# Optimization experiments

Hardware: AMD Instinct MI355X
Metric: run time of the kernel (lower is better)

## Reference

```python
import jax, jax.numpy as jnp
import numpy as np
import math

B, S, H, E, TOPK, NHEADS = 8, 512, 1024, 8, 2, 8
CAP = int(B * S * 1.5 * TOPK / E)  # 1536


def _linear(x, w, b):
    # torch nn.Linear convention: y = x @ w.T + b, w: [out, in]
    return x @ w.T + b


def _mha(x, in_w, in_b, out_w, out_b, n_heads):
    # torch nn.MultiheadAttention self-attention, eval mode (no dropout)
    Bx, Sx, D = x.shape
    dh = D // n_heads
    qkv = x @ in_w.T + in_b                      # [B,S,3D]
    q, k, v = jnp.split(qkv, 3, axis=-1)
    def heads(t):
        return t.reshape(Bx, Sx, n_heads, dh).transpose(0, 2, 1, 3)  # [B,h,S,dh]
    q, k, v = heads(q), heads(k), heads(v)
    scores = jnp.einsum('bhqd,bhkd->bhqk', q, k) / math.sqrt(dh)
    attn = jax.nn.softmax(scores, axis=-1)
    o = jnp.einsum('bhqk,bhkd->bhqd', attn, v)   # [B,h,S,dh]
    o = o.transpose(0, 2, 1, 3).reshape(Bx, Sx, D)
    return o @ out_w.T + out_b


def setup_inputs() -> dict:
    key = jax.random.key(0)
    ks = jax.random.split(key, 24)
    sc = 0.02
    d = {
        'hidden_states': jax.random.normal(ks[0], (B, S, H), jnp.float32),
        'pos_emb': jax.random.normal(ks[1], (S, H), jnp.float32) * sc,
        'se_w1': jax.random.normal(ks[2], (H // 4, 1), jnp.float32) * sc,
        'se_b1': jnp.zeros((H // 4,), jnp.float32),
        'se_w2': jax.random.normal(ks[3], (H // 4, H // 4), jnp.float32) * sc,
        'se_b2': jnp.zeros((H // 4,), jnp.float32),
        'sexp_w': jax.random.normal(ks[4], (H, H // 4), jnp.float32) * sc,
        'sexp_b': jnp.zeros((H,), jnp.float32),
        'te_w1': jax.random.normal(ks[5], (H, H + 2), jnp.float32) * sc,
        'te_b1': jnp.zeros((H,), jnp.float32),
        'te_w2': jax.random.normal(ks[6], (H, H), jnp.float32) * sc,
        'te_b2': jnp.zeros((H,), jnp.float32),
        'attn_in_w': jax.random.normal(ks[7], (3 * H, H), jnp.float32) * sc,
        'attn_in_b': jnp.zeros((3 * H,), jnp.float32),
        'attn_out_w': jax.random.normal(ks[8], (H, H), jnp.float32) * sc,
        'attn_out_b': jnp.zeros((H,), jnp.float32),
        'tr_w1': jax.random.normal(ks[9], (H, H), jnp.float32) * sc,
        'tr_b1': jnp.zeros((H,), jnp.float32),
        'tr_w2': jax.random.normal(ks[10], (E, H), jnp.float32) * sc,
        'tr_b2': jnp.zeros((E,), jnp.float32),
    }
    return d


def reference(hidden_states, pos_emb, se_w1, se_b1, se_w2, se_b2, sexp_w, sexp_b,
              te_w1, te_b1, te_w2, te_b2, attn_in_w, attn_in_b, attn_out_w, attn_out_b,
              tr_w1, tr_b1, tr_w2, tr_b2):
    b, s, h = hidden_states.shape
    timestamps = jnp.arange(s, dtype=hidden_states.dtype)           # [S]
    seasonality = jnp.sin(timestamps * 2 * jnp.pi / 24)             # [S]
    ts_b = jnp.broadcast_to(timestamps, (b, s))
    se_b = jnp.broadcast_to(seasonality, (b, s))

    position_embeddings = pos_emb[:s][None]                          # [1,S,H]
    seas = jax.nn.relu(_linear(se_b[..., None], se_w1, se_b1))       # [B,S,H/4]
    seas = _linear(seas, se_w2, se_b2)
    seasonal_embeddings = _linear(seas, sexp_w, sexp_b)              # [B,S,H]

    time_features = jnp.stack([ts_b, se_b], axis=-1)                 # [B,S,2]
    combined = jnp.concatenate([hidden_states, time_features], -1)   # [B,S,H+2]
    enc = jax.nn.relu(_linear(combined, te_w1, te_b1))
    enc = _linear(enc, te_w2, te_b2)
    enc = enc + position_embeddings + seasonal_embeddings
    enc = _mha(enc, attn_in_w, attn_in_b, attn_out_w, attn_out_b, NHEADS)

    logits = _linear(jax.nn.relu(_linear(enc, tr_w1, tr_b1)), tr_w2, tr_b2)  # [B,S,E]
    router_probs = jax.nn.softmax(logits, axis=-1)
    top_k_probs, top_k_idx = jax.lax.top_k(router_probs, TOPK)
    top_k_probs = top_k_probs / top_k_probs.sum(-1, keepdims=True)

    capacity = int(b * s * 1.5 * TOPK / E)
    # top-k indices are distinct per token, so summed one-hots replicate the
    # python loop's slot-0 writes exactly.
    onehot = jax.nn.one_hot(top_k_idx, E, dtype=router_probs.dtype)  # [B,S,K,E]
    disp0 = onehot.sum(axis=2)                                        # [B,S,E]
    comb0 = jnp.einsum('bske,bsk->bse', onehot, top_k_probs)          # [B,S,E]
    dispatch = jnp.zeros((b, s, E, capacity), router_probs.dtype).at[:, :, :, 0].set(disp0)
    combine = jnp.zeros((b, s, E, capacity), router_probs.dtype).at[:, :, :, 0].set(comb0)

    p_mean = router_probs.mean(axis=(0, 1))
    aux_loss = jnp.sum(p_mean * jnp.log(p_mean * E + 1e-9))
    return dispatch, combine, router_probs, aux_loss
```

## Files before the change

kernel.cpp:

```cpp
#include <hip/hip_runtime.h>
#include <hip/hip_bf16.h>


#define Hh 1024

typedef __attribute__((ext_vector_type(8))) short short8v;
typedef __attribute__((ext_vector_type(4))) float f32x4;

static __device__ __forceinline__ ushort f2bf(float x) {
  uint u = __float_as_uint(x);
  u += 0x7FFF + ((u >> 16) & 1);
  return (ushort)(u >> 16);
}
static __device__ __forceinline__ float bf2f(ushort h) {
  return __uint_as_float(((uint)h) << 16);
}

template<int EPI, bool RELU, bool HAS_BN, bool HAS_BSN>
__global__ __launch_bounds__(256, 2) void mgemm_k(
    const ushort* __restrict__ A, int lda, long long sAmaj, long long sAmin, int aHi, int aLo,
    const ushort* __restrict__ Bf, int BNT, int BKC, long long sBmaj, long long sBmin,
    float* __restrict__ Cf, ushort* __restrict__ Ch, int ldc, long long sCmaj, long long sCmin,
    int splitOff,
    ushort* __restrict__ pK, ushort* __restrict__ pV,
    int Kd, int zdiv,
    const float* __restrict__ bN, const float* __restrict__ bSN, int ldbs, int smod,
    float alpha)
{
  int gx = gridDim.x, gy = gridDim.y;
  int lin = (blockIdx.z * gy + blockIdx.y) * gx + blockIdx.x;
  int nwg = gx * gy * gridDim.z;
  int cpx = nwg >> 3;
  int swz = (lin & 7) * cpx + (lin >> 3);
  int bz = swz / (gx * gy);
  int rem = swz - bz * (gx * gy);
  int by = rem / gx, bx = rem - by * gx;

  int zj = bz / zdiv, zi = bz - zj * zdiv;
  A += (size_t)zj * sAmaj + (size_t)zi * sAmin;
  const ushort* bfb = Bf + (size_t)zj * sBmaj + (size_t)zi * sBmin;
  long long coff = (long long)zj * sCmaj + (long long)zi * sCmin;

  int m0 = by * 128, n0 = bx * 128;

  __shared__ __align__(16) ushort smem[16384];

  int t = threadIdx.x;
  int l = t & 63, w = t >> 6;
  int wm = w >> 1, wn = w & 1;

  f32x4 acc[4][4];
#pragma unroll
  for (int i = 0; i < 4; ++i)
#pragma unroll
    for (int j = 0; j < 4; ++j) acc[i][j] = (f32x4){0.f, 0.f, 0.f, 0.f};

  int srow = t >> 1;
  int sc = (t & 1) * 2;
  const ushort* gAh = A + (size_t)(m0 + srow) * lda + aHi + sc * 8;
  const ushort* gAl = A + (size_t)(m0 + srow) * lda + aLo + sc * 8;
  int wsw = ((srow >> 1) & 7) << 4;
  int wo0 = (srow * 64 + sc * 16) ^ wsw;
  int wo1 = wo0 ^ 16;

  int aoff[4];
#pragma unroll
  for (int mi = 0; mi < 4; ++mi) {
    int row = wm * 64 + mi * 16 + (l & 15);
    aoff[mi] = (row * 64 + (l >> 4) * 16) ^ (((row >> 1) & 7) << 4);
  }

  const ushort* bph[4];
  const ushort* bpl[4];
  int ntg0 = (n0 >> 4) + wn * 4;
#pragma unroll
  for (int ni = 0; ni < 4; ++ni) {
    bph[ni] = bfb + ((size_t)(ntg0 + ni) * BKC) * 512 + l * 8;
    bpl[ni] = bfb + ((size_t)(BNT + ntg0 + ni) * BKC) * 512 + l * 8;
  }

  int4 a0h0, a0h1, a0l0, a0l1, a1h0, a1h1, a1l0, a1l1;
  short8v B0h[4], B0l[4], B1h[4], B1l[4];

#define LOADA0(s) { a0h0 = *(const int4*)(gAh + (s)*32); a0h1 = *(const int4*)(gAh + (s)*32 + 8); \
                    a0l0 = *(const int4*)(gAl + (s)*32); a0l1 = *(const int4*)(gAl + (s)*32 + 8); }
#define LOADA1(s) { a1h0 = *(const int4*)(gAh + (s)*32); a1h1 = *(const int4*)(gAh + (s)*32 + 8); \
                    a1l0 = *(const int4*)(gAl + (s)*32); a1l1 = *(const int4*)(gAl + (s)*32 + 8); }
#define STOREA(h0, h1, l0, l1, base) { char* nb = (char*)smem + (base); \
    *(int4*)(nb + wo0) = h0; *(int4*)(nb + wo1) = h1; \
    *(int4*)(nb + 8192 + wo0) = l0; *(int4*)(nb + 8192 + wo1) = l1; }
#define LOADB(BH, BL, s) { _Pragma("unroll") \
    for (int ni = 0; ni < 4; ++ni) { \
      BH[ni] = *(const short8v*)(bph[ni] + (size_t)(s) * 512); \
      BL[ni] = *(const short8v*)(bpl[ni] + (size_t)(s) * 512); } }
#define MFMA_STEP(ahb, alb, BH, BL) { \
    short8v ah[4], al[4]; \
    _Pragma("unroll") for (int mi = 0; mi < 4; ++mi) \
      ah[mi] = *(const short8v*)((char*)smem + (ahb) + aoff[mi]); \
    _Pragma("unroll") for (int mi = 0; mi < 4; ++mi) \
      al[mi] = *(const short8v*)((char*)smem + (alb) + aoff[mi]); \
    _Pragma("unroll") for (int ni = 0; ni < 4; ++ni) \
      _Pragma("unroll") for (int mi = 0; mi < 4; ++mi) \
        acc[mi][ni] = __builtin_amdgcn_mfma_f32_16x16x32_bf16(ah[mi], BH[ni], acc[mi][ni], 0, 0, 0); \
    _Pragma("unroll") for (int ni = 0; ni < 4; ++ni) \
      _Pragma("unroll") for (int mi = 0; mi < 4; ++mi) \
        acc[mi][ni] = __builtin_amdgcn_mfma_f32_16x16x32_bf16(al[mi], BH[ni], acc[mi][ni], 0, 0, 0); \
    _Pragma("unroll") for (int ni = 0; ni < 4; ++ni) \
      _Pragma("unroll") for (int mi = 0; mi < 4; ++mi) \
        acc[mi][ni] = __builtin_amdgcn_mfma_f32_16x16x32_bf16(ah[mi], BL[ni], acc[mi][ni], 0, 0, 0); }

  int nt = Kd >> 5;
  LOADA0(0); LOADB(B0h, B0l, 0);
  LOADA1(1); LOADB(B1h, B1l, 1);
  STOREA(a0h0, a0h1, a0l0, a0l1, 0);
  __syncthreads();
  for (int s2 = 0; s2 < nt; s2 += 2) {
    if (s2 + 2 < nt) LOADA0(s2 + 2);
    MFMA_STEP(0, 8192, B0h, B0l);
    if (s2 + 2 < nt) LOADB(B0h, B0l, s2 + 2);
    STOREA(a1h0, a1h1, a1l0, a1l1, 16384);
    __syncthreads();
    if (s2 + 3 < nt) LOADA1(s2 + 3);
    MFMA_STEP(16384, 24576, B1h, B1l);
    if (s2 + 3 < nt) LOADB(B1h, B1l, s2 + 3);
    if (s2 + 2 < nt) STOREA(a0h0, a0h1, a0l0, a0l1, 0);
    __syncthreads();
  }
#undef LOADA0
#undef LOADA1
#undef STOREA
#undef LOADB
#undef MFMA_STEP

#pragma unroll
  for (int mi = 0; mi < 4; ++mi)
#pragma unroll
    for (int j = 0; j < 4; ++j) {
      int m = m0 + wm * 64 + mi * 16 + (l >> 4) * 4 + j;
#pragma unroll
      for (int ni = 0; ni < 4; ++ni) {
        int n = n0 + wn * 64 + ni * 16 + (l & 15);
        float x = acc[mi][ni][j] * alpha;
        if (HAS_BN) x += bN[n];
        if (HAS_BSN) x += bSN[(size_t)(m % smod) * ldbs + n];
        if (RELU) x = fmaxf(x, 0.f);
        acc[mi][ni][j] = x;
      }
    }

  if (EPI == 0) {
    float* Fs = (float*)smem;
#pragma unroll
    for (int p = 0; p < 2; ++p) {
      __syncthreads();
      if (wm == p) {
#pragma unroll
        for (int mi = 0; mi < 4; ++mi)
#pragma unroll
          for (int j = 0; j < 4; ++j) {
            int r = mi * 16 + (l >> 4) * 4 + j;
#pragma unroll
            for (int ni = 0; ni < 4; ++ni) {
              int c = wn * 64 + ni * 16 + (l & 15);
              *(float*)((char*)Fs + ((r * 512 + c * 4) ^ ((r & 7) << 4))) = acc[mi][ni][j];
            }
          }
      }
      __syncthreads();
#pragma unroll
      for (int r8 = 0; r8 < 8; ++r8) {
        int idx = r8 * 256 + t;
        int row = idx >> 5, slot = idx & 31;
        int4 v = *(const int4*)((char*)Fs + ((row * 512 + slot * 16) ^ ((row & 7) << 4)));
        *(int4*)(Cf + coff + (size_t)(m0 + p * 64 + row) * ldc + n0 + slot * 4) = v;
      }
    }
  } else {
    __syncthreads();
    ushort* Es = smem;
    bool isQ = (EPI == 1) || (n0 < 1024);
    bool isK = (EPI == 2) && !isQ && (n0 < 2048);
    int bb = m0 >> 9, s0 = m0 & 511;
    int hh2 = isK ? ((n0 - 1024) >> 7) : ((n0 - 2048) >> 7);
    size_t kvb = (size_t)(bb * 8 + hh2) * 131072;
#pragma unroll
    for (int pass = 0; pass < 2; ++pass) {
      if (!(EPI == 2 && !isQ && !isK)) {
#pragma unroll
        for (int mi = 0; mi < 4; ++mi)
#pragma unroll
          for (int j = 0; j < 4; ++j) {
            int lr = wm * 64 + mi * 16 + (l >> 4) * 4 + j;
#pragma unroll
            for (int ni = 0; ni < 4; ++ni) {
              int lcb = (wn * 64 + ni * 16 + (l & 15)) * 2;
              float x = acc[mi][ni][j];
              ushort h = f2bf(x);
              ushort vv = (pass == 0) ? h : f2bf(x - bf2f(h));
              *(ushort*)((char*)Es + ((lr * 256 + lcb) ^ ((lr & 7) << 4))) = vv;
            }
          }
      } else {
#pragma unroll
        for (int mi = 0; mi < 4; ++mi)
#pragma unroll
          for (int j = 0; j < 4; ++j) {
            int cc = (wm * 64 + mi * 16 + (l >> 4) * 4 + j) * 2;
#pragma unroll
            for (int ni = 0; ni < 4; ++ni) {
              int rr = wn * 64 + ni * 16 + (l & 15);
              float x = acc[mi][ni][j];
              ushort h = f2bf(x);
              ushort vv = (pass == 0) ? h : f2bf(x - bf2f(h));
              *(ushort*)((char*)Es + ((rr * 256 + cc) ^ ((rr & 7) << 4))) = vv;
            }
          }
      }
      __syncthreads();
      if (isQ) {
        int off = (pass == 0) ? 0 : splitOff;
#pragma unroll
        for (int r = 0; r < 8; ++r) {
          int idx = r * 256 + t;
          int row = idx >> 4, cb = (idx & 15) * 16;
          int4 v = *(const int4*)((char*)Es + ((row * 256 + cb) ^ ((row & 7) << 4)));
          *(int4*)((char*)(Ch + coff + (size_t)(m0 + row) * ldc + off + n0) + cb) = v;
        }
      } else if (isK) {
#pragma unroll
        for (int sw = 0; sw < 8; ++sw) {
          int idx = sw * 256 + t;
          int f = idx >> 6, l2 = idx & 63;
          int st = f >> 2, dc = f & 3;
          int row = st * 16 + (l2 & 15);
          int colB = (dc * 32 + ((l2 >> 4) << 3)) * 2;
          short8v v = *(const short8v*)((char*)Es + ((row * 256 + colB) ^ ((row & 7) << 4)));
          *(short8v*)(pK + kvb + (size_t)((pass * 32 + (s0 >> 4) + st) * 4 + dc) * 512 + l2 * 8) = v;
        }
      } else {
#pragma unroll
        for (int sw = 0; sw < 8; ++sw) {
          int idx = sw * 256 + t;
          int f = idx >> 6, l2 = idx & 63;
          int dt = f >> 2, sch = f & 3;
          int row = dt * 16 + (l2 & 15);
          int colB = (sch * 32 + ((l2 >> 4) << 3)) * 2;
          short8v v = *(const short8v*)((char*)Es + ((row * 256 + colB) ^ ((row & 7) << 4)));
          *(short8v*)(pV + kvb + (size_t)((pass * 8 + dt) * 16 + (s0 >> 5) + sch) * 512 + l2 * 8) = v;
        }
      }
      if (pass == 0) __syncthreads();
    }
  }
}

__global__ __launch_bounds__(512, 2) void attn_k(
    const ushort* __restrict__ qbuf, const ushort* __restrict__ Kf,
    const ushort* __restrict__ Vf, ushort* __restrict__ attno)
{
  int qt = blockIdx.x;
  int bh = blockIdx.y;
  int b = bh >> 3, h = bh & 7;

  __shared__ __align__(16) ushort smem[32768];
  __shared__ float rowred[1024];

  int t = threadIdx.x;
  int l = t & 63, w = t >> 6;
  int wm = w >> 2, wn = w & 3;

  {
    int srow = t >> 2, sc = t & 3;
    const ushort* gQ = qbuf + (size_t)(b * 512 + qt * 128 + srow) * 2048 + h * 128 + sc * 8;
    int wo = (srow * 64 + sc * 16) ^ (((srow >> 1) & 7) << 4);
#pragma unroll
    for (int ks = 0; ks < 4; ++ks) {
      int4 vh = *(const int4*)(gQ + ks * 32);
      int4 vl = *(const int4*)(gQ + 1024 + ks * 32);
      *(int4*)((char*)smem + ks * 8192 + wo) = vh;
      *(int4*)((char*)smem + 32768 + ks * 8192 + wo) = vl;
    }
  }

  int aoff[4];
#pragma unroll
  for (int mi = 0; mi < 4; ++mi) {
    int row = wm * 64 + mi * 16 + (l & 15);
    aoff[mi] = (row * 64 + (l >> 4) * 16) ^ (((row >> 1) & 7) << 4);
  }

  __syncthreads();

  f32x4 S[4][4][2];
#pragma unroll
  for (int c = 0; c < 4; ++c)
#pragma unroll
    for (int mi = 0; mi < 4; ++mi)
#pragma unroll
      for (int ni = 0; ni < 2; ++ni) S[c][mi][ni] = (f32x4){0.f, 0.f, 0.f, 0.f};

  const ushort* Kb = Kf + (size_t)bh * 131072 + l * 8;
#pragma unroll
  for (int c = 0; c < 4; ++c) {
#pragma unroll
    for (int ks = 0; ks < 4; ++ks) {
      short8v bhf[2], blf[2], ahf[4], alf[4];
#pragma unroll
      for (int ni = 0; ni < 2; ++ni) {
        int ntk = c * 8 + wn * 2 + ni;
        bhf[ni] = *(const short8v*)(Kb + (size_t)(ntk * 4 + ks) * 512);
        blf[ni] = *(const short8v*)(Kb + (size_t)((32 + ntk) * 4 + ks) * 512);
      }
#pragma unroll
      for (int mi = 0; mi < 4; ++mi) {
        ahf[mi] = *(const short8v*)((char*)smem + ks * 8192 + aoff[mi]);
        alf[mi] = *(const short8v*)((char*)smem + 32768 + ks * 8192 + aoff[mi]);
      }
#pragma unroll
      for (int ni = 0; ni < 2; ++ni)
#pragma unroll
        for (int mi = 0; mi < 4; ++mi)
          S[c][mi][ni] = __builtin_amdgcn_mfma_f32_16x16x32_bf16(ahf[mi], bhf[ni], S[c][mi][ni], 0, 0, 0);
#pragma unroll
      for (int ni = 0; ni < 2; ++ni)
#pragma unroll
        for (int mi = 0; mi < 4; ++mi)
          S[c][mi][ni] = __builtin_amdgcn_mfma_f32_16x16x32_bf16(alf[mi], bhf[ni], S[c][mi][ni], 0, 0, 0);
#pragma unroll
      for (int ni = 0; ni < 2; ++ni)
#pragma unroll
        for (int mi = 0; mi < 4; ++mi)
          S[c][mi][ni] = __builtin_amdgcn_mfma_f32_16x16x32_bf16(ahf[mi], blf[ni], S[c][mi][ni], 0, 0, 0);
    }
  }

  const float scale = 0.08838834764831845f;
  float inv16[4][4];
  {
    float mx[4][4];
#pragma unroll
    for (int mi = 0; mi < 4; ++mi)
#pragma unroll
      for (int j = 0; j < 4; ++j) {
        float m2 = -3.0e38f;
#pragma unroll
        for (int c = 0; c < 4; ++c)
#pragma unroll
          for (int ni = 0; ni < 2; ++ni) m2 = fmaxf(m2, S[c][mi][ni][j]);
#pragma unroll
        for (int off = 8; off; off >>= 1) m2 = fmaxf(m2, __shfl_xor(m2, off));
        mx[mi][j] = m2;
      }
    if ((l & 15) == 0) {
#pragma unroll
      for (int mi = 0; mi < 4; ++mi)
#pragma unroll
        for (int j = 0; j < 4; ++j) {
          int row = wm * 64 + mi * 16 + (l >> 4) * 4 + j;
          rowred[wn * 128 + row] = mx[mi][j];
        }
    }
    __syncthreads();
#pragma unroll
    for (int mi = 0; mi < 4; ++mi)
#pragma unroll
      for (int j = 0; j < 4; ++j) {
        int row = wm * 64 + mi * 16 + (l >> 4) * 4 + j;
        float m2 = fmaxf(fmaxf(rowred[row], rowred[128 + row]),
                         fmaxf(rowred[256 + row], rowred[384 + row]));
        mx[mi][j] = m2 * scale;
      }
    float sm[4][4];
#pragma unroll
    for (int mi = 0; mi < 4; ++mi)
#pragma unroll
      for (int j = 0; j < 4; ++j) {
        float s2 = 0.f;
#pragma unroll
        for (int c = 0; c < 4; ++c)
#pragma unroll
          for (int ni = 0; ni < 2; ++ni) {
            float p = __expf(fmaf(S[c][mi][ni][j], scale, -mx[mi][j]));
            S[c][mi][ni][j] = p;
            s2 += p;
          }
#pragma unroll
        for (int off = 8; off; off >>= 1) s2 += __shfl_xor(s2, off);
        sm[mi][j] = s2;
      }
    if ((l & 15) == 0) {
#pragma unroll
      for (int mi = 0; mi < 4; ++mi)
#pragma unroll
        for (int j = 0; j < 4; ++j) {
          int row = wm * 64 + mi * 16 + (l >> 4) * 4 + j;
          rowred[512 + wn * 128 + row] = sm[mi][j];
        }
    }
    __syncthreads();
#pragma unroll
    for (int mi = 0; mi < 4; ++mi)
#pragma unroll
      for (int j = 0; j < 4; ++j) {
        int row = wm * 64 + mi * 16 + (l >> 4) * 4 + j;
        float s2 = rowred[512 + row] + rowred[640 + row]
                 + rowred[768 + row] + rowred[896 + row];
        inv16[mi][j] = 1.f / s2;
      }
  }

  f32x4 O[4][2];
#pragma unroll
  for (int mi = 0; mi < 4; ++mi)
#pragma unroll
    for (int ni = 0; ni < 2; ++ni) O[mi][ni] = (f32x4){0.f, 0.f, 0.f, 0.f};

  const ushort* Vb = Vf + (size_t)bh * 131072 + l * 8;
#pragma unroll
  for (int c = 0; c < 4; ++c) {
    __syncthreads();
#pragma unroll
    for (int mi = 0; mi < 4; ++mi)
#pragma unroll
      for (int j = 0; j < 4; ++j) {
        int row = wm * 64 + mi * 16 + (l >> 4) * 4 + j;
        int sw2 = ((row >> 1) & 7) << 4;
#pragma unroll
        for (int ni = 0; ni < 2; ++ni) {
          float p = S[c][mi][ni][j] * inv16[mi][j];
          ushort hh = f2bf(p);
          ushort ll2 = f2bf(p - bf2f(hh));
          int off = (row * 64 + (ni * 16 + (l & 15)) * 2) ^ sw2;
          *(ushort*)((char*)smem + wn * 8192 + off) = hh;
          *(ushort*)((char*)smem + 32768 + wn * 8192 + off) = ll2;
        }
      }
    __syncthreads();
#pragma unroll
    for (int ks = 0; ks < 4; ++ks) {
      short8v pah[4], pal[4], vbh[2], vbl[2];
#pragma unroll
      for (int ni = 0; ni < 2; ++ni) {
        int ntd = wn * 2 + ni;
        vbh[ni] = *(const short8v*)(Vb + (size_t)(ntd * 16 + c * 4 + ks) * 512);
        vbl[ni] = *(const short8v*)(Vb + (size_t)((8 + ntd) * 16 + c * 4 + ks) * 512);
      }
#pragma unroll
      for (int mi = 0; mi < 4; ++mi) {
        pah[mi] = *(const short8v*)((char*)smem + ks * 8192 + aoff[mi]);
        pal[mi] = *(const short8v*)((char*)smem + 32768 + ks * 8192 + aoff[mi]);
      }
#pragma unroll
      for (int ni = 0; ni < 2; ++ni)
#pragma unroll
        for (int mi = 0; mi < 4; ++mi)
          O[mi][ni] = __builtin_amdgcn_mfma_f32_16x16x32_bf16(pah[mi], vbh[ni], O[mi][ni], 0, 0, 0);
#pragma unroll
      for (int ni = 0; ni < 2; ++ni)
#pragma unroll
        for (int mi = 0; mi < 4; ++mi)
          O[mi][ni] = __builtin_amdgcn_mfma_f32_16x16x32_bf16(pal[mi], vbh[ni], O[mi][ni], 0, 0, 0);
#pragma unroll
      for (int ni = 0; ni < 2; ++ni)
#pragma unroll
        for (int mi = 0; mi < 4; ++mi)
          O[mi][ni] = __builtin_amdgcn_mfma_f32_16x16x32_bf16(pah[mi], vbl[ni], O[mi][ni], 0, 0, 0);
    }
  }

  __syncthreads();
  ushort* Es = smem;
  size_t coff = (size_t)b * 1048576 + (size_t)h * 128;
  int m0 = qt * 128;
#pragma unroll
  for (int pass = 0; pass < 2; ++pass) {
#pragma unroll
    for (int mi = 0; mi < 4; ++mi)
#pragma unroll
      for (int j = 0; j < 4; ++j) {
        int lr = wm * 64 + mi * 16 + (l >> 4) * 4 + j;
#pragma unroll
        for (int ni = 0; ni < 2; ++ni) {
          int lcb = (wn * 32 + ni * 16 + (l & 15)) * 2;
          float x = O[mi][ni][j];
          ushort hh = f2bf(x);
          ushort vv = (pass == 0) ? hh : f2bf(x - bf2f(hh));
          *(ushort*)((char*)Es + ((lr * 256 + lcb) ^ ((lr & 7) << 4))) = vv;
        }
      }
    __syncthreads();
    int off = (pass == 0) ? 0 : 1024;
#pragma unroll
    for (int r = 0; r < 4; ++r) {
      int idx = r * 512 + t;
      int row = idx >> 4, cb = (idx & 15) * 16;
      int4 v = *(const int4*)((char*)Es + ((row * 256 + cb) ^ ((row & 7) << 4)));
      *(int4*)((char*)(attno + coff + (size_t)(m0 + row) * 2048 + off) + cb) = v;
    }
    if (pass == 0) __syncthreads();
  }
}

__global__ __launch_bounds__(64) void convall_k(
    const float* __restrict__ te_w1, const float* __restrict__ te_w2,
    const float* __restrict__ ain_w, const float* __restrict__ aout_w,
    const float* __restrict__ tr_w1, ushort* __restrict__ base)
{
  int kc = blockIdx.x, y = blockIdx.y, l = threadIdx.x;
  const float* W; int ldw, NT, nt2; ushort* dst;
  if (y < 64)       { W = te_w1;  ldw = 1026; NT = 64;  nt2 = y;       dst = base; }
  else if (y < 128) { W = te_w2;  ldw = 1024; NT = 64;  nt2 = y - 64;  dst = base + 2097152; }
  else if (y < 320) { W = ain_w;  ldw = 1024; NT = 192; nt2 = y - 128; dst = base + 4194304; }
  else if (y < 384) { W = aout_w; ldw = 1024; NT = 64;  nt2 = y - 320; dst = base + 10485760; }
  else              { W = tr_w1;  ldw = 1024; NT = 64;  nt2 = y - 384; dst = base + 12582912; }
  const float* src = W + (size_t)(nt2 * 16 + (l & 15)) * ldw + kc * 32 + ((l >> 4) << 3);
  ushort h8[8], l8[8];
#pragma unroll
  for (int j = 0; j < 8; ++j) {
    float x = src[j];
    h8[j] = f2bf(x);
    l8[j] = f2bf(x - bf2f(h8[j]));
  }
  *(int4*)(dst + ((size_t)nt2 * 32 + kc) * 512 + l * 8) = *(int4*)h8;
  *(int4*)(dst + ((size_t)(NT + nt2) * 32 + kc) * 512 + l * 8) = *(int4*)l8;
}

__global__ __launch_bounds__(256) void convert_k(
    const float* __restrict__ W, int lda, ushort* __restrict__ Whl, int K)
{
  int r = blockIdx.x;
  int c = threadIdx.x * 4;
  const float* src = W + (size_t)r * lda + c;
  float x0 = src[0], x1 = src[1], x2 = src[2], x3 = src[3];
  ushort4 h, lo;
  h.x = f2bf(x0); lo.x = f2bf(x0 - bf2f(h.x));
  h.y = f2bf(x1); lo.y = f2bf(x1 - bf2f(h.y));
  h.z = f2bf(x2); lo.z = f2bf(x2 - bf2f(h.z));
  h.w = f2bf(x3); lo.w = f2bf(x3 - bf2f(h.w));
  ushort* dst = Whl + (size_t)r * 2 * K;
  *(ushort4*)&dst[c] = h;
  *(ushort4*)&dst[K + c] = lo;
}

__global__ __launch_bounds__(256) void precompute_k(
    const float* __restrict__ pos_emb,
    const float* __restrict__ se_w1, const float* __restrict__ se_b1,
    const float* __restrict__ se_w2, const float* __restrict__ se_b2,
    const float* __restrict__ sexp_w, const float* __restrict__ sexp_b,
    const float* __restrict__ te_w1, const float* __restrict__ te_b1,
    float* __restrict__ psea, float* __restrict__ bias1)
{
  int s = blockIdx.x, t = threadIdx.x;
  float ts = (float)s;
  float se = sinf(((ts * 2.0f) * 3.14159274101257324f) / 24.0f);
  __shared__ float l1[256], l2[256];
  l1[t] = fmaxf(se * se_w1[t] + se_b1[t], 0.f);
  __syncthreads();
  {
    float a = se_b2[t];
    const float* wr = se_w2 + (size_t)t * 256;
    for (int i = 0; i < 256; ++i) a += l1[i] * wr[i];
    l2[t] = a;
  }
  __syncthreads();
#pragma unroll
  for (int r = 0; r < 4; ++r) {
    int h = r * 256 + t;
    float v = sexp_b[h];
    const float* wr = sexp_w + (size_t)h * 256;
    for (int j = 0; j < 256; ++j) v += l2[j] * wr[j];
    psea[s * Hh + h] = pos_emb[s * Hh + h] + v;
    bias1[s * Hh + h] = te_b1[h] + ts * te_w1[(size_t)h * 1026 + 1024]
                                 + se * te_w1[(size_t)h * 1026 + 1025];
  }
}

__global__ __launch_bounds__(256) void tr2_k(
    const float* __restrict__ h1, const float* __restrict__ w,
    const float* __restrict__ bias, float* __restrict__ logits)
{
  int wid = threadIdx.x >> 6, lane = threadIdx.x & 63;
  int t = blockIdx.x * 4 + wid;
  const float* x = h1 + (size_t)t * Hh;
  float acc[8];
#pragma unroll
  for (int e = 0; e < 8; ++e) acc[e] = 0.f;
  for (int k = lane; k < Hh; k += 64) {
    float xv = x[k];
#pragma unroll
    for (int e = 0; e < 8; ++e) acc[e] += xv * w[e * Hh + k];
  }
#pragma unroll
  for (int e = 0; e < 8; ++e) {
#pragma unroll
    for (int off = 32; off; off >>= 1) acc[e] += __shfl_xor(acc[e], off);
  }
  if (lane == 0) {
#pragma unroll
    for (int e = 0; e < 8; ++e) logits[(size_t)t * 8 + e] = acc[e] + bias[e];
  }
}

__global__ __launch_bounds__(256) void fill0_k(float4* __restrict__ p, long long n4)
{
  long long i = (long long)blockIdx.x * 256 + threadIdx.x;
  long long stride = (long long)gridDim.x * 256;
  float4 z = make_float4(0.f, 0.f, 0.f, 0.f);
  for (; i < n4; i += stride) p[i] = z;
}

__global__ __launch_bounds__(256) void router_k(
    float* __restrict__ out, float* __restrict__ partials)
{
  int t = blockIdx.x * 256 + threadIdx.x;
  float* lg = out + 100663296 + (size_t)t * 8;
  float p[8];
#pragma unroll
  for (int e = 0; e < 8; ++e) p[e] = lg[e];
  float m = p[0];
#pragma unroll
  for (int e = 1; e < 8; ++e) m = fmaxf(m, p[e]);
  float s = 0.f;
#pragma unroll
  for (int e = 0; e < 8; ++e) { p[e] = expf(p[e] - m); s += p[e]; }
  float inv = 1.f / s;
#pragma unroll
  for (int e = 0; e < 8; ++e) p[e] *= inv;
#pragma unroll
  for (int e = 0; e < 8; ++e) lg[e] = p[e];

  int i0 = 0; float v0 = p[0];
#pragma unroll
  for (int e = 1; e < 8; ++e) if (p[e] > v0) { v0 = p[e]; i0 = e; }
  int i1 = -1; float v1 = -1.f;
#pragma unroll
  for (int e = 0; e < 8; ++e) if (e != i0 && p[e] > v1) { v1 = p[e]; i1 = e; }
  float wn = 1.f / (v0 + v1);
  size_t db = (size_t)t * (8 * 1536);
  out[db + (size_t)i0 * 1536] = 1.f;
  out[db + (size_t)i1 * 1536] = 1.f;
  out[50331648 + db + (size_t)i0 * 1536] = v0 * wn;
  out[50331648 + db + (size_t)i1 * 1536] = v1 * wn;

  __shared__ float red[256];
#pragma unroll
  for (int e = 0; e < 8; ++e) {
    red[threadIdx.x] = p[e];
    __syncthreads();
    for (int st = 128; st; st >>= 1) {
      if (threadIdx.x < st) red[threadIdx.x] += red[threadIdx.x + st];
      __syncthreads();
    }
    if (threadIdx.x == 0) partials[blockIdx.x * 8 + e] = red[0];
    __syncthreads();
  }
}

__global__ __launch_bounds__(64) void aux_k(float* __restrict__ partials,
                                            float* __restrict__ out)
{
  int lane = threadIdx.x;
  float v = 0.f;
  if (lane < 8) {
    float s = 0.f;
    for (int b = 0; b < 16; ++b) s += partials[b * 8 + lane];
    float pm = s / 4096.f;
    v = pm * logf(pm * 8.f + 1e-9f);
  }
#pragma unroll
  for (int off = 4; off; off >>= 1) v += __shfl_xor(v, off);
  if (lane == 0) out[100696064] = v;
  partials[lane] = 0.f;
  partials[64 + lane] = 0.f;
}

extern "C" void kernel_launch(void* const* d_in, const int* in_sizes, int n_in,
                              void* d_out, int out_size, void* d_ws, size_t ws_size,
                              hipStream_t stream)
{
  const float* hidden = (const float*)d_in[0];
  const float* pos_emb = (const float*)d_in[1];
  const float* se_w1 = (const float*)d_in[2];
  const float* se_b1 = (const float*)d_in[3];
  const float* se_w2 = (const float*)d_in[4];
  const float* se_b2 = (const float*)d_in[5];
  const float* sexp_w = (const float*)d_in[6];
  const float* sexp_b = (const float*)d_in[7];
  const float* te_w1 = (const float*)d_in[8];
  const float* te_b1 = (const float*)d_in[9];
  const float* te_w2 = (const float*)d_in[10];
  const float* te_b2 = (const float*)d_in[11];
  const float* ain_w = (const float*)d_in[12];
  const float* ain_b = (const float*)d_in[13];
  const float* aout_w = (const float*)d_in[14];
  const float* aout_b = (const float*)d_in[15];
  const float* tr_w1 = (const float*)d_in[16];
  const float* tr_b1 = (const float*)d_in[17];
  const float* tr_w2 = (const float*)d_in[18];
  const float* tr_b2 = (const float*)d_in[19];
  float* out = (float*)d_out;

  char* arena = (char*)d_out;
  ushort* Wbase= (ushort*)(arena + 0);
  ushort* hid2 = (ushort*)(arena + 29360128);
  ushort* enc1 = (ushort*)(arena + 46137344);
  ushort* enc2 = (ushort*)(arena + 62914560);
  ushort* qbuf = (ushort*)(arena + 79691776);
  ushort* Kf   = (ushort*)(arena + 96468992);
  ushort* Vf   = (ushort*)(arena + 113246208);
  ushort* attno= (ushort*)(arena + 197132288);
  ushort* encf = (ushort*)(arena + 213909504);
  float*  h1   = (float*)(arena + 230686720);
  float*  psea = (float*)(arena + 247463936);
  float*  bias1= (float*)(arena + 249561088);
  float*  parts= out + 51380224;
  float*  lgts = out + 100663296;

  convall_k<<<dim3(32, 448), 64, 0, stream>>>(te_w1, te_w2, ain_w, aout_w, tr_w1, Wbase);
  convert_k<<<4096, 256, 0, stream>>>(hidden, 1024, hid2, 1024);
  precompute_k<<<512, 256, 0, stream>>>(pos_emb, se_w1, se_b1, se_w2, se_b2,
                                        sexp_w, sexp_b, te_w1, te_b1, psea, bias1);

  mgemm_k<1, true, false, true><<<dim3(8, 32, 1), 256, 0, stream>>>(
      hid2, 2048, 0, 0, 0, 1024,
      Wbase, 64, 32, 0, 0,
      nullptr, enc1, 2048, 0, 0, 1024, nullptr, nullptr,
      1024, 1, nullptr, bias1, 1024, 512, 1.f);

  mgemm_k<1, false, true, true><<<dim3(8, 32, 1), 256, 0, stream>>>(
      enc1, 2048, 0, 0, 0, 1024,
      Wbase + 2097152, 64, 32, 0, 0,
      nullptr, enc2, 2048, 0, 0, 1024, nullptr, nullptr,
      1024, 1, te_b2, psea, 1024, 512, 1.f);

  mgemm_k<2, false, true, false><<<dim3(24, 32, 1), 256, 0, stream>>>(
      enc2, 2048, 0, 0, 0, 1024,
      Wbase + 4194304, 192, 32, 0, 0,
      nullptr, qbuf, 2048, 0, 0, 1024, Kf, Vf,
      1024, 1, ain_b, nullptr, 1, 1, 1.f);

  attn_k<<<dim3(4, 64), 512, 0, stream>>>(qbuf, Kf, Vf, attno);

  mgemm_k<1, false, true, false><<<dim3(8, 32, 1), 256, 0, stream>>>(
      attno, 2048, 0, 0, 0, 1024,
      Wbase + 10485760, 64, 32, 0, 0,
      nullptr, encf, 2048, 0, 0, 1024, nullptr, nullptr,
      1024, 1, aout_b, nullptr, 1, 1, 1.f);

  mgemm_k<0, true, true, false><<<dim3(8, 32, 1), 256, 0, stream>>>(
      encf, 2048, 0, 0, 0, 1024,
      Wbase + 12582912, 64, 32, 0, 0,
      h1, nullptr, 1024, 0, 0, 0, nullptr, nullptr,
      1024, 1, tr_b1, nullptr, 1, 1, 1.f);

  tr2_k<<<1024, 256, 0, stream>>>(h1, tr_w2, tr_b2, lgts);

  fill0_k<<<4096, 256, 0, stream>>>((float4*)out, 25165824LL);

  router_k<<<16, 256, 0, stream>>>(out, parts);
  aux_k<<<1, 64, 0, stream>>>(parts, out);
}
```

Measured before the change: 460.4 us.

## Spread output zero-fill across GEMM, attention and router kernels as extra blocks

The separate zero-fill kernel for the large dispatch/combine output is split into 256KB chunks. Each chunk is written by extra workgroups appended to the grids of the GEMM, attention and tr2 kernels, using arena regions that are free at that point in the schedule. The intent is to overlap the memory-bound fill with compute-bound kernels instead of running it serially. The cost is extra grid blocks that compete for CUs, and a dependency on careful arena aliasing so no buffer that is still live gets zeroed.

```diff
diff --git a/kernel.cpp b/kernel.cpp
--- a/kernel.cpp
+++ b/kernel.cpp
@@ -14,6 +14,18 @@
 }
 static __device__ __forceinline__ float bf2f(ushort h) {
   return __uint_as_float(((uint)h) << 16);
+}
+
+static __device__ __forceinline__ void fill_chunk(char* fz, long long base,
+                                                  long long limit, long long id) {
+  long long zo = base + id * 262144LL;
+  if (zo < limit) {
+    long long n16 = (limit - zo) >> 4;
+    if (n16 > 16384) n16 = 16384;
+    float4* zp = (float4*)(fz + zo);
+    float4 zz = make_float4(0.f, 0.f, 0.f, 0.f);
+    for (long long i = threadIdx.x; i < n16; i += blockDim.x) zp[i] = zz;
+  }
 }
 
 template<int EPI, bool RELU, bool HAS_BN, bool HAS_BSN>
@@ -25,9 +37,17 @@
     ushort* __restrict__ pK, ushort* __restrict__ pV,
     int Kd, int zdiv,
     const float* __restrict__ bN, const float* __restrict__ bSN, int ldbs, int smod,
-    float alpha)
-{
-  int gx = gridDim.x, gy = gridDim.y;
+    float alpha,
+    char* __restrict__ fz, long long fzBase, long long fzLimit, int gemmGX)
+{
+  int gy = gridDim.y;
+  if ((int)blockIdx.x >= gemmGX) {
+    int fx = gridDim.x - gemmGX;
+    long long id = ((long long)blockIdx.z * gy + blockIdx.y) * fx + (blockIdx.x - gemmGX);
+    fill_chunk(fz, fzBase, fzLimit, id);
+    return;
+  }
+  int gx = gemmGX;
   int lin = (blockIdx.z * gy + blockIdx.y) * gx + blockIdx.x;
   int nwg = gx * gy * gridDim.z;
   int cpx = nwg >> 3;
@@ -256,8 +276,13 @@
 
 __global__ __launch_bounds__(512, 2) void attn_k(
     const ushort* __restrict__ qbuf, const ushort* __restrict__ Kf,
-    const ushort* __restrict__ Vf, ushort* __restrict__ attno)
-{
+    const ushort* __restrict__ Vf, ushort* __restrict__ attno,
+    char* __restrict__ fz, long long fzBase, long long fzLimit)
+{
+  if (blockIdx.x >= 4) {
+    fill_chunk(fz, fzBase, fzLimit, (long long)blockIdx.y);
+    return;
+  }
   int qt = blockIdx.x;
   int bh = blockIdx.y;
   int b = bh >> 3, h = bh & 7;
@@ -577,8 +602,16 @@
 
 __global__ __launch_bounds__(256) void tr2_k(
     const float* __restrict__ h1, const float* __restrict__ w,
-    const float* __restrict__ bias, float* __restrict__ logits)
-{
+    const float* __restrict__ bias, float* __restrict__ logits,
+    char* __restrict__ fz, long long baseA, long long limitA,
+    long long baseB, long long limitB, int nA)
+{
+  if ((int)blockIdx.x >= 1024) {
+    int id = blockIdx.x - 1024;
+    if (id < nA) fill_chunk(fz, baseA, limitA, id);
+    else fill_chunk(fz, baseB, limitB, id - nA);
+    return;
+  }
   int wid = threadIdx.x >> 6, lane = threadIdx.x & 63;
   int t = blockIdx.x * 4 + wid;
   const float* x = h1 + (size_t)t * Hh;
@@ -721,41 +754,49 @@
   precompute_k<<<512, 256, 0, stream>>>(pos_emb, se_w1, se_b1, se_w2, se_b2,
                                         sexp_w, sexp_b, te_w1, te_b1, psea, bias1);
 
-  mgemm_k<1, true, false, true><<<dim3(8, 32, 1), 256, 0, stream>>>(
+  mgemm_k<1, true, false, true><<<dim3(16, 32, 1), 256, 0, stream>>>(
       hid2, 2048, 0, 0, 0, 1024,
       Wbase, 64, 32, 0, 0,
       nullptr, enc1, 2048, 0, 0, 1024, nullptr, nullptr,
-      1024, 1, nullptr, bias1, 1024, 512, 1.f);
-
-  mgemm_k<1, false, true, true><<<dim3(8, 32, 1), 256, 0, stream>>>(
+      1024, 1, nullptr, bias1, 1024, 512, 1.f,
+      arena, 130023424LL, 197132288LL, 8);
+
+  mgemm_k<1, false, true, true><<<dim3(16, 32, 1), 256, 0, stream>>>(
       enc1, 2048, 0, 0, 0, 1024,
       Wbase + 2097152, 64, 32, 0, 0,
       nullptr, enc2, 2048, 0, 0, 1024, nullptr, nullptr,
-      1024, 1, te_b2, psea, 1024, 512, 1.f);
-
-  mgemm_k<2, false, true, false><<<dim3(24, 32, 1), 256, 0, stream>>>(
+      1024, 1, te_b2, psea, 1024, 512, 1.f,
+      arena, 251658240LL, 318767104LL, 8);
+
+  mgemm_k<2, false, true, false><<<dim3(32, 32, 1), 256, 0, stream>>>(
       enc2, 2048, 0, 0, 0, 1024,
       Wbase + 4194304, 192, 32, 0, 0,
       nullptr, qbuf, 2048, 0, 0, 1024, Kf, Vf,
-      1024, 1, ain_b, nullptr, 1, 1, 1.f);
-
-  attn_k<<<dim3(4, 64), 512, 0, stream>>>(qbuf, Kf, Vf, attno);
-
-  mgemm_k<1, false, true, false><<<dim3(8, 32, 1), 256, 0, stream>>>(
+      1024, 1, ain_b, nullptr, 1, 1, 1.f,
+      arena, 318767104LL, 385875968LL, 24);
+
+  attn_k<<<dim3(5, 64), 512, 0, stream>>>(qbuf, Kf, Vf, attno,
+                                          arena, 385875968LL, 402653184LL);
+
+  mgemm_k<1, false, true, false><<<dim3(14, 32, 1), 256, 0, stream>>>(
       attno, 2048, 0, 0, 0, 1024,
       Wbase + 10485760, 64, 32, 0, 0,
       nullptr, encf, 2048, 0, 0, 1024, nullptr, nullptr,
-      1024, 1, aout_b, nullptr, 1, 1, 1.f);
-
-  mgemm_k<0, true, true, false><<<dim3(8, 32, 1), 256, 0, stream>>>(
+      1024, 1, aout_b, nullptr, 1, 1, 1.f,
+      arena, 79691776LL, 130023424LL, 8);
+
+  mgemm_k<0, true, true, false><<<dim3(14, 32, 1), 256, 0, stream>>>(
       encf, 2048, 0, 0, 0, 1024,
       Wbase + 12582912, 64, 32, 0, 0,
       h1, nullptr, 1024, 0, 0, 0, nullptr, nullptr,
-      1024, 1, tr_b1, nullptr, 1, 1, 1.f);
-
-  tr2_k<<<1024, 256, 0, stream>>>(h1, tr_w2, tr_b2, lgts);
-
-  fill0_k<<<4096, 256, 0, stream>>>((float4*)out, 25165824LL);
+      1024, 1, tr_b1, nullptr, 1, 1, 1.f,
+      arena, 29360128LL, 79691776LL, 8);
+
+  tr2_k<<<1264, 256, 0, stream>>>(h1, tr_w2, tr_b2, lgts,
+                                  arena, 0LL, 29360128LL,
+                                  197132288LL, 230686720LL, 112);
+
+  fill0_k<<<80, 256, 0, stream>>>((float4*)(arena + 230686720), 1310720LL);
 
   router_k<<<16, 256, 0, stream>>>(out, parts);
   aux_k<<<1, 64, 0, stream>>>(parts, out);
```

Result: slower. 552.6 us (+20.0%).

## Double the GEMM K-tile to 64 to halve barriers per K step

Applied to the files above, without the earlier changes.

The split-bf16 GEMM mainloop now stages 64-wide K tiles of A (hi and lo) in LDS instead of 32-wide. It uses a new XOR swizzle and issues two MFMA sub-steps per barrier, so there is one __syncthreads per 64 K. This cuts synchronization and LDS store overhead per MFMA. In exchange it doubles LDS to 64KB per block and adds more A staging registers, which may reduce occupancy below the two-blocks-per-CU launch bound. It also assumes K is a multiple of 128.

```diff
diff --git a/kernel.cpp b/kernel.cpp
--- a/kernel.cpp
+++ b/kernel.cpp
@@ -43,7 +43,7 @@
 
   int m0 = by * 128, n0 = bx * 128;
 
-  __shared__ __align__(16) ushort smem[16384];
+  __shared__ __align__(16) ushort smem[32768];
 
   int t = threadIdx.x;
   int l = t & 63, w = t >> 6;
@@ -56,18 +56,21 @@
     for (int j = 0; j < 4; ++j) acc[i][j] = (f32x4){0.f, 0.f, 0.f, 0.f};
 
   int srow = t >> 1;
-  int sc = (t & 1) * 2;
-  const ushort* gAh = A + (size_t)(m0 + srow) * lda + aHi + sc * 8;
-  const ushort* gAl = A + (size_t)(m0 + srow) * lda + aLo + sc * 8;
-  int wsw = ((srow >> 1) & 7) << 4;
-  int wo0 = (srow * 64 + sc * 16) ^ wsw;
-  int wo1 = wo0 ^ 16;
-
-  int aoff[4];
+  int sc4 = (t & 1) * 4;
+  const ushort* gAh = A + (size_t)(m0 + srow) * lda + aHi + sc4 * 8;
+  const ushort* gAl = A + (size_t)(m0 + srow) * lda + aLo + sc4 * 8;
+  int woA[4];
+#pragma unroll
+  for (int i = 0; i < 4; ++i)
+    woA[i] = srow * 128 + (((sc4 + i) ^ (srow & 7)) << 4);
+
+  int aoff[4][2];
 #pragma unroll
   for (int mi = 0; mi < 4; ++mi) {
     int row = wm * 64 + mi * 16 + (l & 15);
-    aoff[mi] = (row * 64 + (l >> 4) * 16) ^ (((row >> 1) & 7) << 4);
+#pragma unroll
+    for (int kk = 0; kk < 2; ++kk)
+      aoff[mi][kk] = row * 128 + ((((kk << 2) + (l >> 4)) ^ (row & 7)) << 4);
   }
 
   const ushort* bph[4];
@@ -79,26 +82,29 @@
     bpl[ni] = bfb + ((size_t)(BNT + ntg0 + ni) * BKC) * 512 + l * 8;
   }
 
-  int4 a0h0, a0h1, a0l0, a0l1, a1h0, a1h1, a1l0, a1l1;
+  int4 a0h[4], a0l[4], a1h[4], a1l[4];
   short8v B0h[4], B0l[4], B1h[4], B1l[4];
 
-#define LOADA0(s) { a0h0 = *(const int4*)(gAh + (s)*32); a0h1 = *(const int4*)(gAh + (s)*32 + 8); \
-                    a0l0 = *(const int4*)(gAl + (s)*32); a0l1 = *(const int4*)(gAl + (s)*32 + 8); }
-#define LOADA1(s) { a1h0 = *(const int4*)(gAh + (s)*32); a1h1 = *(const int4*)(gAh + (s)*32 + 8); \
-                    a1l0 = *(const int4*)(gAl + (s)*32); a1l1 = *(const int4*)(gAl + (s)*32 + 8); }
-#define STOREA(h0, h1, l0, l1, base) { char* nb = (char*)smem + (base); \
-    *(int4*)(nb + wo0) = h0; *(int4*)(nb + wo1) = h1; \
-    *(int4*)(nb + 8192 + wo0) = l0; *(int4*)(nb + 8192 + wo1) = l1; }
-#define LOADB(BH, BL, s) { _Pragma("unroll") \
+#define LOADA0(tile) { _Pragma("unroll") for (int i = 0; i < 4; ++i) { \
+    a0h[i] = *(const int4*)(gAh + (tile) * 64 + i * 8); \
+    a0l[i] = *(const int4*)(gAl + (tile) * 64 + i * 8); } }
+#define LOADA1(tile) { _Pragma("unroll") for (int i = 0; i < 4; ++i) { \
+    a1h[i] = *(const int4*)(gAh + (tile) * 64 + i * 8); \
+    a1l[i] = *(const int4*)(gAl + (tile) * 64 + i * 8); } }
+#define STOREA(ah, al, base) { char* nb = (char*)smem + (base); \
+    _Pragma("unroll") for (int i = 0; i < 4; ++i) { \
+      *(int4*)(nb + woA[i]) = ah[i]; \
+      *(int4*)(nb + 16384 + woA[i]) = al[i]; } }
+#define LOADB(BH, BL, chunk) { _Pragma("unroll") \
     for (int ni = 0; ni < 4; ++ni) { \
-      BH[ni] = *(const short8v*)(bph[ni] + (size_t)(s) * 512); \
-      BL[ni] = *(const short8v*)(bpl[ni] + (size_t)(s) * 512); } }
-#define MFMA_STEP(ahb, alb, BH, BL) { \
+      BH[ni] = *(const short8v*)(bph[ni] + (size_t)(chunk) * 512); \
+      BL[ni] = *(const short8v*)(bpl[ni] + (size_t)(chunk) * 512); } }
+#define MFMA64(ahb, kk, BH, BL) { \
     short8v ah[4], al[4]; \
     _Pragma("unroll") for (int mi = 0; mi < 4; ++mi) \
-      ah[mi] = *(const short8v*)((char*)smem + (ahb) + aoff[mi]); \
+      ah[mi] = *(const short8v*)((char*)smem + (ahb) + aoff[mi][kk]); \
     _Pragma("unroll") for (int mi = 0; mi < 4; ++mi) \
-      al[mi] = *(const short8v*)((char*)smem + (alb) + aoff[mi]); \
+      al[mi] = *(const short8v*)((char*)smem + (ahb) + 16384 + aoff[mi][kk]); \
     _Pragma("unroll") for (int ni = 0; ni < 4; ++ni) \
       _Pragma("unroll") for (int mi = 0; mi < 4; ++mi) \
         acc[mi][ni] = __builtin_amdgcn_mfma_f32_16x16x32_bf16(ah[mi], BH[ni], acc[mi][ni], 0, 0, 0); \
@@ -109,28 +115,33 @@
       _Pragma("unroll") for (int mi = 0; mi < 4; ++mi) \
         acc[mi][ni] = __builtin_amdgcn_mfma_f32_16x16x32_bf16(ah[mi], BL[ni], acc[mi][ni], 0, 0, 0); }
 
-  int nt = Kd >> 5;
-  LOADA0(0); LOADB(B0h, B0l, 0);
-  LOADA1(1); LOADB(B1h, B1l, 1);
-  STOREA(a0h0, a0h1, a0l0, a0l1, 0);
+  int nk = Kd >> 5;
+  int nt64 = Kd >> 6;
+  LOADA0(0); LOADB(B0h, B0l, 0); LOADB(B1h, B1l, 1);
+  LOADA1(1);
+  STOREA(a0h, a0l, 0);
   __syncthreads();
-  for (int s2 = 0; s2 < nt; s2 += 2) {
-    if (s2 + 2 < nt) LOADA0(s2 + 2);
-    MFMA_STEP(0, 8192, B0h, B0l);
-    if (s2 + 2 < nt) LOADB(B0h, B0l, s2 + 2);
-    STOREA(a1h0, a1h1, a1l0, a1l1, 16384);
-    __syncthreads();
-    if (s2 + 3 < nt) LOADA1(s2 + 3);
-    MFMA_STEP(16384, 24576, B1h, B1l);
-    if (s2 + 3 < nt) LOADB(B1h, B1l, s2 + 3);
-    if (s2 + 2 < nt) STOREA(a0h0, a0h1, a0l0, a0l1, 0);
+  for (int tt = 0; tt < nt64; tt += 2) {
+    if (tt + 2 < nt64) LOADA0(tt + 2);
+    MFMA64(0, 0, B0h, B0l);
+    if (2 * tt + 2 < nk) LOADB(B0h, B0l, 2 * tt + 2);
+    MFMA64(0, 1, B1h, B1l);
+    if (2 * tt + 3 < nk) LOADB(B1h, B1l, 2 * tt + 3);
+    STOREA(a1h, a1l, 32768);
+    __syncthreads();
+    if (tt + 3 < nt64) LOADA1(tt + 3);
+    MFMA64(32768, 0, B0h, B0l);
+    if (2 * tt + 4 < nk) LOADB(B0h, B0l, 2 * tt + 4);
+    MFMA64(32768, 1, B1h, B1l);
+    if (2 * tt + 5 < nk) LOADB(B1h, B1l, 2 * tt + 5);
+    if (tt + 2 < nt64) STOREA(a0h, a0l, 0);
     __syncthreads();
   }
 #undef LOADA0
 #undef LOADA1
 #undef STOREA
 #undef LOADB
-#undef MFMA_STEP
+#undef MFMA64
 
 #pragma unroll
   for (int mi = 0; mi < 4; ++mi)
```

Measured after the change: 671.6 us. +45.9%, slower.
